# Kernel tuning notes

Measured on AMD Instinct MI355X. Metric: run time of the kernel, lower is better.

Reference implementation:

```python
import jax, jax.numpy as jnp
import numpy as np

EMBED_DIM = 768
NUM_HEADS = 12
HEAD_DIM = EMBED_DIM // NUM_HEADS


def setup_inputs() -> dict:
    key = jax.random.key(0)
    k_x, k_wqkv, k_bqkv, k_wp, k_bp = jax.random.split(key, 5)
    B, N, C = 2, 2048, EMBED_DIM
    lim_qkv = 1.0 / np.sqrt(C)
    lim_p = 1.0 / np.sqrt(C)
    return {
        "x": jax.random.normal(k_x, (B, N, C), dtype=jnp.float32),
        # torch Linear weights: [out_features, in_features]
        "w_qkv": jax.random.uniform(k_wqkv, (3 * C, C), minval=-lim_qkv, maxval=lim_qkv, dtype=jnp.float32),
        "b_qkv": jax.random.uniform(k_bqkv, (3 * C,), minval=-lim_qkv, maxval=lim_qkv, dtype=jnp.float32),
        "w_proj": jax.random.uniform(k_wp, (C, C), minval=-lim_p, maxval=lim_p, dtype=jnp.float32),
        "b_proj": jax.random.uniform(k_bp, (C,), minval=-lim_p, maxval=lim_p, dtype=jnp.float32),
    }


def reference(x, w_qkv, b_qkv, w_proj, b_proj):
    b, n, c = x.shape
    h, d = NUM_HEADS, HEAD_DIM
    qkv = x @ w_qkv.T + b_qkv                      # [b, n, 3c]
    qkv = qkv.reshape(b, n, 3, h, d).transpose(2, 0, 3, 1, 4)  # [3, b, h, n, d]
    q, k, v = qkv[0], qkv[1], qkv[2]
    scale = d ** -0.5
    attn = jnp.einsum('bhnd,bhmd->bhnm', q, k) * scale  # [b, h, n, n]
    attn = jax.nn.softmax(attn, axis=-1)
    # dropout is identity at inference (eval mode)
    out = jnp.einsum('bhnm,bhmd->bhnd', attn, v)        # [b, h, n, d]
    out = out.transpose(0, 2, 1, 3).reshape(b, n, c)    # [b, n, c]
    return out @ w_proj.T + b_proj
```

## Files before the change

### kernel.cpp

```cpp
#include <hip/hip_runtime.h>
#include <cstdint>
#include <cstddef>

using u16    = uint16_t;
using u16x4  = __attribute__((ext_vector_type(4))) uint16_t;
using u16x8  = __attribute__((ext_vector_type(8))) uint16_t;
using bf16x2 = __attribute__((ext_vector_type(2))) __bf16;
using bf16x8 = __attribute__((ext_vector_type(8))) __bf16;
using f32x4  = __attribute__((ext_vector_type(4))) float;
using f32x16 = __attribute__((ext_vector_type(16))) float;

__device__ __forceinline__ u16 f2b(float f) {
    union { float f; uint32_t u; } x; x.f = f;
    uint32_t r = x.u + 0x7FFFu + ((x.u >> 16) & 1u);
    return (u16)(r >> 16);
}
__device__ __forceinline__ uint32_t pk2(float a, float b) {
    bf16x2 t; t[0] = (__bf16)a; t[1] = (__bf16)b;
    return __builtin_bit_cast(uint32_t, t);
}
__device__ __forceinline__ u16x8 ld8u(const u16* p) {
    union { u16x8 v; u16x4 h[2]; } r;
    r.h[0] = *(const u16x4*)p;
    r.h[1] = *(const u16x4*)(p + 4);
    return r.v;
}
__device__ __forceinline__ float ex2(float x) {
#if __has_builtin(__builtin_amdgcn_exp2f)
    return __builtin_amdgcn_exp2f(x);
#else
    return __expf(x * 0.6931471805599453f);
#endif
}

__device__ __forceinline__ void load16_async(const u16* g, u16* lds_base) {
    __builtin_amdgcn_global_load_lds(
        (const __attribute__((address_space(1))) u16*)g,
        (__attribute__((address_space(3))) u16*)(uint32_t)(uintptr_t)lds_base,
        16, 0, 0);
}

__global__ void conv_k(const float* __restrict__ x,  u16* __restrict__ xb,  int nx4,
                       const float* __restrict__ w1, u16* __restrict__ w1b, int n14,
                       const float* __restrict__ w2, u16* __restrict__ w2b, int n24)
{
    const int t   = blockIdx.x * blockDim.x + threadIdx.x;
    const int stp = gridDim.x * blockDim.x;
    for (int i = t; i < nx4; i += stp) {
        f32x4 v = ((const f32x4*)x)[i];
        u16x4 o;
        #pragma unroll
        for (int e = 0; e < 4; e++) o[e] = f2b(v[e]);
        ((u16x4*)xb)[i] = o;
    }
    for (int i = t; i < n14; i += stp) {
        f32x4 v = ((const f32x4*)w1)[i];
        u16x4 o;
        #pragma unroll
        for (int e = 0; e < 4; e++) o[e] = f2b(v[e]);
        ((u16x4*)w1b)[i] = o;
    }
    for (int i = t; i < n24; i += stp) {
        f32x4 v = ((const f32x4*)w2)[i];
        u16x4 o;
        #pragma unroll
        for (int e = 0; e < 4; e++) o[e] = f2b(v[e]);
        ((u16x4*)w2b)[i] = o;
    }
}

__global__ __launch_bounds__(256, 3) void gemm_qkv(
    const u16* __restrict__ A, const u16* __restrict__ W,
    const float* __restrict__ bias,
    u16* __restrict__ O0, u16* __restrict__ Kt, u16* __restrict__ Vt)
{
    __shared__ alignas(16) char smem[33792];
    u16* As = (u16*)smem;
    u16* Bs = (u16*)(smem + 16384);
    u16* T  = (u16*)smem;

    const int tid  = threadIdx.x;
    const int wid  = tid >> 6, lane = tid & 63;
    const int quad = lane >> 4, lc = lane & 15;
    const int row0 = blockIdx.x * 128, col0 = blockIdx.y * 128;
    const int wm   = (wid >> 1) * 64, wn = (wid & 1) * 64;

    const int srA = wid * 8 + (lane >> 3);
    const int scA = ((lane & 7) ^ ((lane >> 3) & 7)) * 8;
    const int rc0 = ((0*4 + quad) ^ (lc & 7)) * 8;
    const int rc1 = ((1*4 + quad) ^ (lc & 7)) * 8;

    f32x4 acc[4][4] = {};

    for (int k0 = 0; k0 < 768; k0 += 64) {
        __syncthreads();
        #pragma unroll
        for (int c = 0; c < 4; c++) {
            load16_async(&A[(row0 + c*32 + srA) * 768 + k0 + scA], &As[(c*32 + wid*8) * 64]);
            load16_async(&W[(col0 + c*32 + srA) * 768 + k0 + scA], &Bs[(c*32 + wid*8) * 64]);
        }
        __syncthreads();

        #pragma unroll
        for (int s = 0; s < 2; s++) {
            const int rc = s ? rc1 : rc0;
            bf16x8 a[4], b[4];
            #pragma unroll
            for (int i = 0; i < 4; i++)
                a[i] = __builtin_bit_cast(bf16x8, *(const u16x8*)&As[(wm + i*16 + lc)*64 + rc]);
            #pragma unroll
            for (int j = 0; j < 4; j++)
                b[j] = __builtin_bit_cast(bf16x8, *(const u16x8*)&Bs[(wn + j*16 + lc)*64 + rc]);
            #pragma unroll
            for (int i = 0; i < 4; i++)
                #pragma unroll
                for (int j = 0; j < 4; j++)
                    acc[i][j] = __builtin_amdgcn_mfma_f32_16x16x32_bf16(a[i], b[j], acc[i][j], 0, 0, 0);
        }
    }

    if (col0 < 768) {
        #pragma unroll
        for (int i = 0; i < 4; i++) {
            #pragma unroll
            for (int j = 0; j < 4; j++) {
                const int gc = col0 + wn + j*16 + lc;
                const float bv = bias[gc];
                #pragma unroll
                for (int r = 0; r < 4; r++) {
                    const int gr = row0 + wm + i*16 + quad*4 + r;
                    O0[gr * 768 + gc] = f2b(acc[i][j][r] + bv);
                }
            }
        }
    } else if (col0 < 1536) {
        __syncthreads();
        u16* T2 = T;
        #pragma unroll
        for (int j = 0; j < 4; j++) {
            const int fl = wn + j*16 + lc;
            const float bv = bias[col0 + fl];
            #pragma unroll
            for (int i = 0; i < 4; i++)
                #pragma unroll
                for (int r = 0; r < 4; r++)
                    T2[(wm + i*16 + quad*4 + r)*132 + fl] = f2b(acc[i][j][r] + bv);
        }
        __syncthreads();

        const int t7 = tid & 127, hloc = tid >> 7;
        const int bh = (row0 >> 11) * 12 + ((col0 - 768) >> 6) + hloc;
        const int kg0 = (row0 & 2047) >> 5;
        u16* dst = Kt + (size_t)bh * 131072 + (size_t)kg0 * 2048;
        #pragma unroll
        for (int i = 0; i < 8; i++) {
            const int idx = t7 + 128*i;
            const int lr = idx & 31, hl = (idx >> 5) & 1;
            const int c  = (idx >> 6) & 3, lkg = idx >> 8;
            const u16* src = &T2[(lkg*32 + lr)*132 + hloc*64 + c*16 + hl*8];
            *(u16x8*)&dst[lkg*2048 + c*512 + hl*256 + lr*8] = ld8u(src);
        }
    } else {
        __syncthreads();
        #pragma unroll
        for (int j = 0; j < 4; j++) {
            const int cl = wn + j*16 + lc;
            const float bv = bias[col0 + cl];
            #pragma unroll
            for (int i = 0; i < 4; i++) {
                uint2 w;
                w.x = pk2(acc[i][j][0] + bv, acc[i][j][1] + bv);
                w.y = pk2(acc[i][j][2] + bv, acc[i][j][3] + bv);
                *(uint2*)&T[cl*132 + wm + i*16 + quad*4] = w;
            }
        }
        __syncthreads();

        const int t7 = tid & 127, hloc = tid >> 7;
        const int bh = (row0 >> 11) * 12 + ((col0 - 1536) >> 6) + hloc;
        const int kg0 = (row0 & 2047) >> 5;
        u16* dst = Vt + (size_t)bh * 131072 + (size_t)kg0 * 2048;
        #pragma unroll
        for (int i = 0; i < 8; i++) {
            const int idx = t7 + 128*i;
            const int L = idx & 63, f = (idx >> 6) & 3, lkg = idx >> 8;
            const int lr = L & 31, hl = L >> 5;
            const u16* src = &T[(hloc*64 + (f>>1)*32 + lr)*132 + lkg*32 + (f&1)*16 + hl*4];
            union { u16x8 v; u16x4 h[2]; } rr;
            rr.h[0] = *(const u16x4*)src;
            rr.h[1] = *(const u16x4*)(src + 8);
            *(u16x8*)&dst[lkg*2048 + f*512 + L*8] = rr.v;
        }
    }
}

__global__ __launch_bounds__(256, 4) void gemm_proj(
    const u16* __restrict__ A, const u16* __restrict__ W,
    const float* __restrict__ bias, float* __restrict__ F0)
{
    __shared__ alignas(16) u16 As[64 * 64];
    __shared__ alignas(16) u16 Bs[64 * 64];
    const int tid  = threadIdx.x;
    const int wid  = tid >> 6, lane = tid & 63;
    const int quad = lane >> 4, lc = lane & 15;
    const int row0 = blockIdx.x * 64, col0 = blockIdx.y * 64;
    const int wm   = (wid >> 1) * 32, wn = (wid & 1) * 32;

    const int srA = wid * 8 + (lane >> 3);
    const int scA = ((lane & 7) ^ ((lane >> 3) & 7)) * 8;
    const int rc0 = ((0*4 + quad) ^ (lc & 7)) * 8;
    const int rc1 = ((1*4 + quad) ^ (lc & 7)) * 8;

    f32x4 acc[2][2] = {};

    for (int k0 = 0; k0 < 768; k0 += 64) {
        __syncthreads();
        #pragma unroll
        for (int c = 0; c < 2; c++) {
            load16_async(&A[(row0 + c*32 + srA) * 768 + k0 + scA], &As[(c*32 + wid*8) * 64]);
            load16_async(&W[(col0 + c*32 + srA) * 768 + k0 + scA], &Bs[(c*32 + wid*8) * 64]);
        }
        __syncthreads();

        #pragma unroll
        for (int s = 0; s < 2; s++) {
            const int rc = s ? rc1 : rc0;
            bf16x8 a[2], b[2];
            #pragma unroll
            for (int i = 0; i < 2; i++)
                a[i] = __builtin_bit_cast(bf16x8, *(const u16x8*)&As[(wm + i*16 + lc)*64 + rc]);
            #pragma unroll
            for (int j = 0; j < 2; j++)
                b[j] = __builtin_bit_cast(bf16x8, *(const u16x8*)&Bs[(wn + j*16 + lc)*64 + rc]);
            #pragma unroll
            for (int i = 0; i < 2; i++)
                #pragma unroll
                for (int j = 0; j < 2; j++)
                    acc[i][j] = __builtin_amdgcn_mfma_f32_16x16x32_bf16(a[i], b[j], acc[i][j], 0, 0, 0);
        }
    }

    #pragma unroll
    for (int i = 0; i < 2; i++)
        #pragma unroll
        for (int j = 0; j < 2; j++) {
            const int gc = col0 + wn + j*16 + lc;
            const float bv = bias[gc];
            #pragma unroll
            for (int r = 0; r < 4; r++) {
                const int gr = row0 + wm + i*16 + quad*4 + r;
                F0[gr * 768 + gc] = acc[i][j][r] + bv;
            }
        }
}

__global__ __launch_bounds__(256, 3) void attn_k(
    const u16* __restrict__ Q, const u16* __restrict__ Kt,
    const u16* __restrict__ Vt, u16* __restrict__ O)
{
    __shared__ alignas(16) char lds[34304];
    float* Obuf = (float*)lds;
    float* Lbuf = (float*)(lds + 33792);

    const int tid  = threadIdx.x;
    const int wid  = tid >> 6, lane = tid & 63;
    const int hl   = lane >> 5;
    const int lr   = lane & 31;
    const int li = blockIdx.x;
    const int bh = li >> 5, qt = li & 31;
    const int b = bh / 12, h = bh - b * 12;
    const int q0 = qt * 64;

    const u16* Qp = Q + ((size_t)b * 2048) * 768 + h * 64;
    u16*       Op = O + ((size_t)b * 2048) * 768 + h * 64;
    const u16* Kb = Kt + (size_t)bh * 131072;
    const u16* Vb = Vt + (size_t)bh * 131072;
    const int lo8 = lane * 8;

    const float qs = 0.125f * 1.4426950408889634f;
    bf16x8 qf[2][4];
    #pragma unroll
    for (int qh = 0; qh < 2; qh++)
        #pragma unroll
        for (int c = 0; c < 4; c++) {
            u16x8 t = *(const u16x8*)&Qp[(q0 + qh*32 + lr) * 768 + c*16 + hl*8];
            bf16x8 sc;
            #pragma unroll
            for (int e = 0; e < 8; e++) {
                union { uint32_t u; float f; } z; z.u = ((uint32_t)t[e]) << 16;
                sc[e] = (__bf16)(z.f * qs);
            }
            qf[qh][c] = sc;
        }

    float l0 = 0.f, l1 = 0.f;
    f32x16 o00 = {}, o01 = {}, o10 = {}, o11 = {};

    bf16x8 kreg[4];
    #pragma unroll
    for (int c = 0; c < 4; c++)
        kreg[c] = __builtin_bit_cast(bf16x8, *(const u16x8*)&Kb[wid*2048 + c*512 + lo8]);

    for (int kt = 0; kt < 16; kt++) {
        const int kg = kt*4 + wid;
        const u16* vt = &Vb[(size_t)kg * 2048 + lo8];
        u16x8 va0r = *(const u16x8*)&vt[0];
        u16x8 va1r = *(const u16x8*)&vt[512];
        u16x8 vb0r = *(const u16x8*)&vt[1024];
        u16x8 vb1r = *(const u16x8*)&vt[1536];

        f32x16 s = {};
        __builtin_amdgcn_s_setprio(1);
        #pragma unroll
        for (int c = 0; c < 4; c++)
            s = __builtin_amdgcn_mfma_f32_32x32x16_bf16(kreg[c], qf[0][c], s, 0, 0, 0);
        __builtin_amdgcn_s_setprio(0);

        #pragma unroll
        for (int r = 0; r < 16; r++) {
            float p = ex2(s[r]);
            s[r] = p;
            l0 += p;
        }
        union { bf16x8 v; uint32_t w[4]; } pA, pB;
        #pragma unroll
        for (int e2 = 0; e2 < 4; e2++) {
            pA.w[e2] = pk2(s[2*e2],     s[2*e2 + 1]);
            pB.w[e2] = pk2(s[8 + 2*e2], s[8 + 2*e2 + 1]);
        }
        {
            bf16x8 va0 = __builtin_bit_cast(bf16x8, va0r);
            bf16x8 va1 = __builtin_bit_cast(bf16x8, va1r);
            bf16x8 vb0 = __builtin_bit_cast(bf16x8, vb0r);
            bf16x8 vb1 = __builtin_bit_cast(bf16x8, vb1r);
            __builtin_amdgcn_s_setprio(1);
            o00 = __builtin_amdgcn_mfma_f32_32x32x16_bf16(va0, pA.v, o00, 0, 0, 0);
            o00 = __builtin_amdgcn_mfma_f32_32x32x16_bf16(va1, pB.v, o00, 0, 0, 0);
            o01 = __builtin_amdgcn_mfma_f32_32x32x16_bf16(vb0, pA.v, o01, 0, 0, 0);
            o01 = __builtin_amdgcn_mfma_f32_32x32x16_bf16(vb1, pB.v, o01, 0, 0, 0);
            __builtin_amdgcn_s_setprio(0);
        }

        f32x16 t = {};
        __builtin_amdgcn_s_setprio(1);
        #pragma unroll
        for (int c = 0; c < 4; c++)
            t = __builtin_amdgcn_mfma_f32_32x32x16_bf16(kreg[c], qf[1][c], t, 0, 0, 0);
        __builtin_amdgcn_s_setprio(0);

        if (kt < 15) {
            #pragma unroll
            for (int c = 0; c < 4; c++)
                kreg[c] = __builtin_bit_cast(bf16x8, *(const u16x8*)&Kb[(size_t)(kg + 4)*2048 + c*512 + lo8]);
        }

        #pragma unroll
        for (int r = 0; r < 16; r++) {
            float p = ex2(t[r]);
            t[r] = p;
            l1 += p;
        }
        union { bf16x8 v; uint32_t w[4]; } pC, pD;
        #pragma unroll
        for (int e2 = 0; e2 < 4; e2++) {
            pC.w[e2] = pk2(t[2*e2],     t[2*e2 + 1]);
            pD.w[e2] = pk2(t[8 + 2*e2], t[8 + 2*e2 + 1]);
        }
        {
            bf16x8 va0 = __builtin_bit_cast(bf16x8, va0r);
            bf16x8 va1 = __builtin_bit_cast(bf16x8, va1r);
            bf16x8 vb0 = __builtin_bit_cast(bf16x8, vb0r);
            bf16x8 vb1 = __builtin_bit_cast(bf16x8, vb1r);
            __builtin_amdgcn_s_setprio(1);
            o10 = __builtin_amdgcn_mfma_f32_32x32x16_bf16(va0, pC.v, o10, 0, 0, 0);
            o10 = __builtin_amdgcn_mfma_f32_32x32x16_bf16(va1, pD.v, o10, 0, 0, 0);
            o11 = __builtin_amdgcn_mfma_f32_32x32x16_bf16(vb0, pC.v, o11, 0, 0, 0);
            o11 = __builtin_amdgcn_mfma_f32_32x32x16_bf16(vb1, pD.v, o11, 0, 0, 0);
            __builtin_amdgcn_s_setprio(0);
        }
    }

    l0 += __shfl_xor(l0, 32);
    l1 += __shfl_xor(l1, 32);

    const int q  = tid & 31;
    const int dblk = tid >> 5;

    if (lane < 32) Lbuf[wid*32 + lr] = l0;
    #pragma unroll
    for (int r = 0; r < 16; r++) {
        const int dr = (r & 3) + 8*(r >> 2) + 4*hl;
        Obuf[(wid*64 + dr)*33 + lr]      = o00[r];
        Obuf[(wid*64 + 32 + dr)*33 + lr] = o01[r];
    }
    __syncthreads();
    {
        const float linv = 1.0f / (Lbuf[q] + Lbuf[32 + q] + Lbuf[64 + q] + Lbuf[96 + q]);
        u16x8 ov;
        #pragma unroll
        for (int j = 0; j < 8; j++) {
            const int d = dblk*8 + j;
            const float sum = Obuf[(0*64 + d)*33 + q] + Obuf[(1*64 + d)*33 + q] +
                              Obuf[(2*64 + d)*33 + q] + Obuf[(3*64 + d)*33 + q];
            ov[j] = f2b(sum * linv);
        }
        *(u16x8*)&Op[(size_t)(q0 + q) * 768 + dblk*8] = ov;
    }
    __syncthreads();

    if (lane < 32) Lbuf[wid*32 + lr] = l1;
    #pragma unroll
    for (int r = 0; r < 16; r++) {
        const int dr = (r & 3) + 8*(r >> 2) + 4*hl;
        Obuf[(wid*64 + dr)*33 + lr]      = o10[r];
        Obuf[(wid*64 + 32 + dr)*33 + lr] = o11[r];
    }
    __syncthreads();
    {
        const float linv = 1.0f / (Lbuf[q] + Lbuf[32 + q] + Lbuf[64 + q] + Lbuf[96 + q]);
        u16x8 ov;
        #pragma unroll
        for (int j = 0; j < 8; j++) {
            const int d = dblk*8 + j;
            const float sum = Obuf[(0*64 + d)*33 + q] + Obuf[(1*64 + d)*33 + q] +
                              Obuf[(2*64 + d)*33 + q] + Obuf[(3*64 + d)*33 + q];
            ov[j] = f2b(sum * linv);
        }
        *(u16x8*)&Op[(size_t)(q0 + 32 + q) * 768 + dblk*8] = ov;
    }
}

extern "C" void kernel_launch(void* const* d_in, const int* in_sizes, int n_in,
                              void* d_out, int out_size, void* d_ws, size_t ws_size,
                              hipStream_t stream)
{
    const float* x    = (const float*)d_in[0];
    const float* wqkv = (const float*)d_in[1];
    const float* bqkv = (const float*)d_in[2];
    const float* wp   = (const float*)d_in[3];
    const float* bp   = (const float*)d_in[4];
    float* out = (float*)d_out;
    char* ws = (char*)d_ws;

    u16* Qw    = (u16*)(ws);
    u16* Vt    = (u16*)(ws + 6291456);
    u16* wqkvb = (u16*)(ws + 12582912);
    u16* wpb   = (u16*)(ws + 16121856);
    u16* Kt    = (u16*)d_out;
    u16* xb    = (u16*)((char*)d_out + 6291456);

    conv_k<<<512, 256, 0, stream>>>(x, xb, 3145728/4, wqkv, wqkvb, 1769472/4, wp, wpb, 589824/4);
    gemm_qkv<<<dim3(32, 18), 256, 0, stream>>>(xb, wqkvb, bqkv, Qw, Kt, Vt);
    attn_k<<<768, 256, 0, stream>>>(Qw, Kt, Vt, Qw);
    gemm_proj<<<dim3(64, 12), 256, 0, stream>>>(Qw, wpb, bp, out);
}
```

Before: 137.6 us.

## Double-buffer K and V register prefetch two tiles ahead in attention loop

The attention main loop now keeps two register sets of K and V tiles and prefetches both two iterations ahead, replacing the previous scheme where K was prefetched one tile ahead and V was loaded at the top of each iteration. This hides global-load latency for V behind MFMA work. The extra registers force launch bounds to drop from 3 to 2 waves-per-block occupancy hint. Prefetch indices wrap modulo 16, so the last iterations issue redundant loads.

```diff
diff --git a/kernel.cpp b/kernel.cpp
--- a/kernel.cpp
+++ b/kernel.cpp
@@ -254,7 +254,71 @@
         }
 }
 
-__global__ __launch_bounds__(256, 3) void attn_k(
+#define ATT_ITER(KS, VS, NXT)                                                 \
+    {                                                                         \
+        f32x16 s = {};                                                        \
+        __builtin_amdgcn_s_setprio(1);                                        \
+        _Pragma("unroll")                                                     \
+        for (int c = 0; c < 4; c++)                                           \
+            s = __builtin_amdgcn_mfma_f32_32x32x16_bf16(                      \
+                    __builtin_bit_cast(bf16x8, KS[c]), qf[0][c], s, 0, 0, 0); \
+        __builtin_amdgcn_s_setprio(0);                                        \
+        _Pragma("unroll")                                                     \
+        for (int r = 0; r < 16; r++) {                                        \
+            float p = ex2(s[r]); s[r] = p; l0 += p;                           \
+        }                                                                     \
+        union { bf16x8 v; uint32_t w[4]; } pA, pB;                            \
+        _Pragma("unroll")                                                     \
+        for (int e2 = 0; e2 < 4; e2++) {                                      \
+            pA.w[e2] = pk2(s[2*e2],     s[2*e2 + 1]);                         \
+            pB.w[e2] = pk2(s[8 + 2*e2], s[8 + 2*e2 + 1]);                     \
+        }                                                                     \
+        __builtin_amdgcn_s_setprio(1);                                        \
+        o00 = __builtin_amdgcn_mfma_f32_32x32x16_bf16(                        \
+                  __builtin_bit_cast(bf16x8, VS[0]), pA.v, o00, 0, 0, 0);     \
+        o00 = __builtin_amdgcn_mfma_f32_32x32x16_bf16(                        \
+                  __builtin_bit_cast(bf16x8, VS[1]), pB.v, o00, 0, 0, 0);     \
+        o01 = __builtin_amdgcn_mfma_f32_32x32x16_bf16(                        \
+                  __builtin_bit_cast(bf16x8, VS[2]), pA.v, o01, 0, 0, 0);     \
+        o01 = __builtin_amdgcn_mfma_f32_32x32x16_bf16(                        \
+                  __builtin_bit_cast(bf16x8, VS[3]), pB.v, o01, 0, 0, 0);     \
+        __builtin_amdgcn_s_setprio(0);                                        \
+        f32x16 t2 = {};                                                       \
+        __builtin_amdgcn_s_setprio(1);                                        \
+        _Pragma("unroll")                                                     \
+        for (int c = 0; c < 4; c++)                                           \
+            t2 = __builtin_amdgcn_mfma_f32_32x32x16_bf16(                     \
+                    __builtin_bit_cast(bf16x8, KS[c]), qf[1][c], t2, 0, 0, 0);\
+        __builtin_amdgcn_s_setprio(0);                                        \
+        _Pragma("unroll")                                                     \
+        for (int c = 0; c < 4; c++)                                           \
+            KS[c] = *(const u16x8*)&Kb[(size_t)(NXT)*2048 + c*512 + lo8];     \
+        _Pragma("unroll")                                                     \
+        for (int r = 0; r < 16; r++) {                                        \
+            float p = ex2(t2[r]); t2[r] = p; l1 += p;                         \
+        }                                                                     \
+        union { bf16x8 v; uint32_t w[4]; } pC, pD;                            \
+        _Pragma("unroll")                                                     \
+        for (int e2 = 0; e2 < 4; e2++) {                                      \
+            pC.w[e2] = pk2(t2[2*e2],     t2[2*e2 + 1]);                       \
+            pD.w[e2] = pk2(t2[8 + 2*e2], t2[8 + 2*e2 + 1]);                   \
+        }                                                                     \
+        __builtin_amdgcn_s_setprio(1);                                        \
+        o10 = __builtin_amdgcn_mfma_f32_32x32x16_bf16(                        \
+                  __builtin_bit_cast(bf16x8, VS[0]), pC.v, o10, 0, 0, 0);     \
+        o10 = __builtin_amdgcn_mfma_f32_32x32x16_bf16(                        \
+                  __builtin_bit_cast(bf16x8, VS[1]), pD.v, o10, 0, 0, 0);     \
+        o11 = __builtin_amdgcn_mfma_f32_32x32x16_bf16(                        \
+                  __builtin_bit_cast(bf16x8, VS[2]), pC.v, o11, 0, 0, 0);     \
+        o11 = __builtin_amdgcn_mfma_f32_32x32x16_bf16(                        \
+                  __builtin_bit_cast(bf16x8, VS[3]), pD.v, o11, 0, 0, 0);     \
+        __builtin_amdgcn_s_setprio(0);                                        \
+        _Pragma("unroll")                                                     \
+        for (int c = 0; c < 4; c++)                                           \
+            VS[c] = *(const u16x8*)&Vb[(size_t)(NXT)*2048 + c*512 + lo8];     \
+    }
+
+__global__ __launch_bounds__(256, 2) void attn_k(
     const u16* __restrict__ Q, const u16* __restrict__ Kt,
     const u16* __restrict__ Vt, u16* __restrict__ O)
 {
@@ -296,88 +360,18 @@
     float l0 = 0.f, l1 = 0.f;
     f32x16 o00 = {}, o01 = {}, o10 = {}, o11 = {};
 
-    bf16x8 kreg[4];
+    u16x8 kA[4], kB[4], vA[4], vB[4];
     #pragma unroll
-    for (int c = 0; c < 4; c++)
-        kreg[c] = __builtin_bit_cast(bf16x8, *(const u16x8*)&Kb[wid*2048 + c*512 + lo8]);
-
-    for (int kt = 0; kt < 16; kt++) {
-        const int kg = kt*4 + wid;
-        const u16* vt = &Vb[(size_t)kg * 2048 + lo8];
-        u16x8 va0r = *(const u16x8*)&vt[0];
-        u16x8 va1r = *(const u16x8*)&vt[512];
-        u16x8 vb0r = *(const u16x8*)&vt[1024];
-        u16x8 vb1r = *(const u16x8*)&vt[1536];
-
-        f32x16 s = {};
-        __builtin_amdgcn_s_setprio(1);
-        #pragma unroll
-        for (int c = 0; c < 4; c++)
-            s = __builtin_amdgcn_mfma_f32_32x32x16_bf16(kreg[c], qf[0][c], s, 0, 0, 0);
-        __builtin_amdgcn_s_setprio(0);
-
-        #pragma unroll
-        for (int r = 0; r < 16; r++) {
-            float p = ex2(s[r]);
-            s[r] = p;
-            l0 += p;
-        }
-        union { bf16x8 v; uint32_t w[4]; } pA, pB;
-        #pragma unroll
-        for (int e2 = 0; e2 < 4; e2++) {
-            pA.w[e2] = pk2(s[2*e2],     s[2*e2 + 1]);
-            pB.w[e2] = pk2(s[8 + 2*e2], s[8 + 2*e2 + 1]);
-        }
-        {
-            bf16x8 va0 = __builtin_bit_cast(bf16x8, va0r);
-            bf16x8 va1 = __builtin_bit_cast(bf16x8, va1r);
-            bf16x8 vb0 = __builtin_bit_cast(bf16x8, vb0r);
-            bf16x8 vb1 = __builtin_bit_cast(bf16x8, vb1r);
-            __builtin_amdgcn_s_setprio(1);
-            o00 = __builtin_amdgcn_mfma_f32_32x32x16_bf16(va0, pA.v, o00, 0, 0, 0);
-            o00 = __builtin_amdgcn_mfma_f32_32x32x16_bf16(va1, pB.v, o00, 0, 0, 0);
-            o01 = __builtin_amdgcn_mfma_f32_32x32x16_bf16(vb0, pA.v, o01, 0, 0, 0);
-            o01 = __builtin_amdgcn_mfma_f32_32x32x16_bf16(vb1, pB.v, o01, 0, 0, 0);
-            __builtin_amdgcn_s_setprio(0);
-        }
-
-        f32x16 t = {};
-        __builtin_amdgcn_s_setprio(1);
-        #pragma unroll
-        for (int c = 0; c < 4; c++)
-            t = __builtin_amdgcn_mfma_f32_32x32x16_bf16(kreg[c], qf[1][c], t, 0, 0, 0);
-        __builtin_amdgcn_s_setprio(0);
-
-        if (kt < 15) {
-            #pragma unroll
-            for (int c = 0; c < 4; c++)
-                kreg[c] = __builtin_bit_cast(bf16x8, *(const u16x8*)&Kb[(size_t)(kg + 4)*2048 + c*512 + lo8]);
-        }
-
-        #pragma unroll
-        for (int r = 0; r < 16; r++) {
-            float p = ex2(t[r]);
-            t[r] = p;
-            l1 += p;
-        }
-        union { bf16x8 v; uint32_t w[4]; } pC, pD;
-        #pragma unroll
-        for (int e2 = 0; e2 < 4; e2++) {
-            pC.w[e2] = pk2(t[2*e2],     t[2*e2 + 1]);
-            pD.w[e2] = pk2(t[8 + 2*e2], t[8 + 2*e2 + 1]);
-        }
-        {
-            bf16x8 va0 = __builtin_bit_cast(bf16x8, va0r);
-            bf16x8 va1 = __builtin_bit_cast(bf16x8, va1r);
-            bf16x8 vb0 = __builtin_bit_cast(bf16x8, vb0r);
-            bf16x8 vb1 = __builtin_bit_cast(bf16x8, vb1r);
-            __builtin_amdgcn_s_setprio(1);
-            o10 = __builtin_amdgcn_mfma_f32_32x32x16_bf16(va0, pC.v, o10, 0, 0, 0);
-            o10 = __builtin_amdgcn_mfma_f32_32x32x16_bf16(va1, pD.v, o10, 0, 0, 0);
-            o11 = __builtin_amdgcn_mfma_f32_32x32x16_bf16(vb0, pC.v, o11, 0, 0, 0);
-            o11 = __builtin_amdgcn_mfma_f32_32x32x16_bf16(vb1, pD.v, o11, 0, 0, 0);
-            __builtin_amdgcn_s_setprio(0);
-        }
+    for (int c = 0; c < 4; c++) {
+        kA[c] = *(const u16x8*)&Kb[(size_t)(0*4 + wid)*2048 + c*512 + lo8];
+        vA[c] = *(const u16x8*)&Vb[(size_t)(0*4 + wid)*2048 + c*512 + lo8];
+        kB[c] = *(const u16x8*)&Kb[(size_t)(1*4 + wid)*2048 + c*512 + lo8];
+        vB[c] = *(const u16x8*)&Vb[(size_t)(1*4 + wid)*2048 + c*512 + lo8];
+    }
+
+    for (int kt = 0; kt < 16; kt += 2) {
+        ATT_ITER(kA, vA, (((kt + 2) & 15) * 4 + wid));
+        ATT_ITER(kB, vB, (((kt + 3) & 15) * 4 + wid));
     }
 
     l0 += __shfl_xor(l0, 32);
```

Result: no change. 136.7 us (-0.7%).
